# Kernel tuning notes

Measured on AMD Instinct MI355X. Metric: run time of the kernel, lower is better.

The kernel has to match this reference:

```python
import jax, jax.numpy as jnp
import numpy as np

N = 20000
E = 320000
IN_DIM = 16
H = 128
HEADS = 4
NEG_SLOPE = 0.2  # GATv2Conv default
EPS_LN = 1e-5


def setup_inputs() -> dict:
    key = jax.random.key(0)
    ks = jax.random.split(key, 16)
    f32 = jnp.float32
    def rn(k, shape, scale):
        return jax.random.normal(k, shape, dtype=f32) * scale
    s_in = 1.0 / np.sqrt(IN_DIM)
    s_h = 1.0 / np.sqrt(H)
    s_4h = 1.0 / np.sqrt(4 * H)
    s_2h = 1.0 / np.sqrt(2 * H)
    inp = {}
    inp["x"] = jax.random.normal(ks[0], (N, IN_DIM), dtype=f32)
    inp["edge_index"] = jax.random.randint(ks[1], (2, E), 0, N)
    inp["edge_attr"] = jax.random.normal(ks[2], (E, 2), dtype=f32)
    inp["emb_w"] = rn(ks[3], (IN_DIM, H), s_in)
    inp["emb_b"] = jnp.zeros((H,), f32)
    # 3 GATv2 layers stacked on leading axis
    inp["lin_l"] = rn(ks[4], (3, H, HEADS * H), s_h)
    inp["lin_r"] = rn(ks[5], (3, H, HEADS * H), s_h)
    inp["lin_edge"] = rn(ks[6], (3, 2, HEADS * H), 1.0 / np.sqrt(2.0))
    inp["att"] = rn(ks[7], (3, HEADS, H), s_h)
    inp["conv_bias01"] = jnp.zeros((2, HEADS * H), f32)  # concat=True layers
    inp["conv_bias2"] = jnp.zeros((H,), f32)             # concat=False layer
    inp["proj_w"] = rn(ks[8], (2, HEADS * H, H), s_4h)
    inp["proj_b"] = jnp.zeros((2, H), f32)
    inp["n1_g"] = jnp.ones((3, H), f32)
    inp["n1_b"] = jnp.zeros((3, H), f32)
    inp["n2_g"] = jnp.ones((3, H), f32)
    inp["n2_b"] = jnp.zeros((3, H), f32)
    inp["ffn_w1"] = rn(ks[9], (3, H, 2 * H), s_h)
    inp["ffn_b1"] = jnp.zeros((3, 2 * H), f32)
    inp["ffn_w2"] = rn(ks[10], (3, 2 * H, H), s_2h)
    inp["ffn_b2"] = jnp.zeros((3, H), f32)
    return inp


def layer_norm(x, g, b):
    mu = jnp.mean(x, axis=-1, keepdims=True)
    var = jnp.mean((x - mu) ** 2, axis=-1, keepdims=True)
    return (x - mu) * jax.lax.rsqrt(var + EPS_LN) * g + b


def gatv2(h, src, dst, eattr, Wl, Wr, We, att, bias, concat, n):
    # h: [n, H]; per-edge gather -> GATv2 attention -> segment softmax -> scatter-add
    xl = (h @ Wl).reshape(n, HEADS, H)   # source transform
    xr = (h @ Wr).reshape(n, HEADS, H)   # target transform
    ee = (eattr @ We).reshape(-1, HEADS, H)
    e = jax.nn.leaky_relu(xl[src] + xr[dst] + ee, NEG_SLOPE)  # [E', HEADS, H]
    score = jnp.einsum('ehc,hc->eh', e, att)                  # [E', HEADS]
    smax = jax.ops.segment_max(score, dst, num_segments=n)
    p = jnp.exp(score - smax[dst])
    denom = jax.ops.segment_sum(p, dst, num_segments=n)
    alpha = p / (denom[dst] + 1e-16)
    out = jax.ops.segment_sum(xl[src] * alpha[..., None], dst, num_segments=n)
    if concat:
        return out.reshape(n, HEADS * H) + bias
    return jnp.mean(out, axis=1) + bias


def reference(x, edge_index, edge_attr, emb_w, emb_b, lin_l, lin_r, lin_edge, att,
              conv_bias01, conv_bias2, proj_w, proj_b, n1_g, n1_b, n2_g, n2_b,
              ffn_w1, ffn_b1, ffn_w2, ffn_b2):
    n = x.shape[0]
    e = edge_attr.shape[0]
    # PyG add_self_loops with fill_value='mean': self-loop attr = mean of incoming edge attrs
    ones = jnp.ones((e,), x.dtype)
    deg = jax.ops.segment_sum(ones, edge_index[1], num_segments=n)
    loop_attr = jax.ops.segment_sum(edge_attr, edge_index[1], num_segments=n) / jnp.maximum(deg, 1.0)[:, None]
    ar = jnp.arange(n)
    src = jnp.concatenate([edge_index[0], ar])
    dst = jnp.concatenate([edge_index[1], ar])
    ea = jnp.concatenate([edge_attr, loop_attr], axis=0)

    h = x @ emb_w + emb_b
    for i in range(3):
        concat = i < 2
        bias = conv_bias01[i] if concat else conv_bias2
        h_in = h
        h = gatv2(h, src, dst, ea, lin_l[i], lin_r[i], lin_edge[i], att[i], bias, concat, n)
        if concat:
            h = h @ proj_w[i] + proj_b[i]
        h = layer_norm(h + h_in, n1_g[i], n1_b[i])
        h2 = h
        h = jax.nn.gelu(h @ ffn_w1[i] + ffn_b1[i], approximate=False) @ ffn_w2[i] + ffn_b2[i]
        h = layer_norm(h + h2, n2_g[i], n2_b[i])
    return h
```

## Files before the change

kernel.cpp:

```cpp
#include <hip/hip_runtime.h>
#include <math.h>

#define IN_DIM 16
#define HDIM   128
#define HEADS  4
#define HH     512
#define FFH    256
#define NEG_SLOPE 0.2f

typedef _Float16 half8 __attribute__((ext_vector_type(8)));
typedef _Float16 h8 __attribute__((ext_vector_type(8)));
typedef _Float16 h4 __attribute__((ext_vector_type(4)));
typedef _Float16 h2 __attribute__((ext_vector_type(2)));
typedef float f32x4 __attribute__((ext_vector_type(4)));
typedef int i32x4 __attribute__((ext_vector_type(4)));

struct __align__(8) Edge { int src; _Float16 ea0, ea1; };

static __device__ inline float hsum8(h8 v) {
    h4 a = __builtin_shufflevector(v, v, 0, 1, 2, 3) +
           __builtin_shufflevector(v, v, 4, 5, 6, 7);
    h2 b = __builtin_shufflevector(a, a, 0, 1) +
           __builtin_shufflevector(a, a, 2, 3);
    return (float)b[0] + (float)b[1];
}

static __device__ inline h8 shfl_xor_h8(h8 v, int off) {
    union { h8 h; i32x4 i; } u;
    u.h = v;
    u.i.x = __shfl_xor(u.i.x, off);
    u.i.y = __shfl_xor(u.i.y, off);
    u.i.z = __shfl_xor(u.i.z, off);
    u.i.w = __shfl_xor(u.i.w, off);
    return u.h;
}

__global__ void xpad_kernel(const float* __restrict__ x, _Float16* __restrict__ xh, int n) {
    int idx = blockIdx.x * 256 + threadIdx.x;
    if (idx >= n * 64) return;
    int r = idx >> 6, k = idx & 63;
    xh[idx] = (k < IN_DIM) ? (_Float16)x[r * IN_DIM + k] : (_Float16)0.0f;
}

struct WDesc { const float* src; _Float16* dst; int Ksrc; int lgKd; int lgN; };
struct WDescs { WDesc d[15]; };
__global__ void wconv_kernel(WDescs ds) {
    WDesc w = ds.d[blockIdx.y];
    int Kd = 1 << w.lgKd;
    int total = 1 << (w.lgKd + w.lgN);
    for (int idx = blockIdx.x * 256 + threadIdx.x; idx < total; idx += gridDim.x * 256) {
        int n2 = idx >> w.lgKd, k = idx & (Kd - 1);
        w.dst[idx] = (k < w.Ksrc) ? (_Float16)w.src[(k << w.lgN) + n2] : (_Float16)0.0f;
    }
}

__global__ void wcvt_kernel(const float* __restrict__ we, const float* __restrict__ att,
                            const float* __restrict__ cb,
                            _Float16* __restrict__ weh, _Float16* __restrict__ atth,
                            _Float16* __restrict__ cbh) {
    int i = blockIdx.x * 256 + threadIdx.x;
    if (i < 3072) weh[i] = (_Float16)we[i];
    else if (i < 4608) atth[i - 3072] = (_Float16)att[i - 3072];
    else if (i < 5632) cbh[i - 4608] = (_Float16)cb[i - 4608];
}

__global__ void deg_kernel(const int* __restrict__ ei, const float* __restrict__ eattr,
                           float* deg, float* asum, int E) {
    int e = blockIdx.x * blockDim.x + threadIdx.x;
    if (e >= E) return;
    int d = ei[E + e];
    atomicAdd(&deg[d], 1.0f);
    atomicAdd(&asum[2 * d], eattr[2 * e]);
    atomicAdd(&asum[2 * d + 1], eattr[2 * e + 1]);
}

__global__ void scan_kernel(const float* __restrict__ deg, int* row_ptr, int* cur, int n) {
    __shared__ int sums[1024];
    int tid = threadIdx.x;
    int per = (n + 1023) / 1024;
    int s0 = tid * per;
    int s1 = s0 + per; if (s1 > n) s1 = n;
    int s = 0;
    for (int i = s0; i < s1; i++) s += (int)deg[i] + 1;
    int mysum = s;
    sums[tid] = s;
    __syncthreads();
    for (int dd = 1; dd < 1024; dd <<= 1) {
        int t = (tid >= dd) ? sums[tid - dd] : 0;
        __syncthreads();
        sums[tid] += t;
        __syncthreads();
    }
    int run = sums[tid] - mysum;
    for (int i = s0; i < s1; i++) {
        row_ptr[i] = run; cur[i] = run;
        run += (int)deg[i] + 1;
    }
    if (tid == 1023) row_ptr[n] = sums[1023];
}

__global__ void scatter_kernel(const int* __restrict__ ei, const float* __restrict__ eattr,
                               const float* __restrict__ deg, const float* __restrict__ asum,
                               int* cur, Edge* csr, int E, int n) {
    int i = blockIdx.x * blockDim.x + threadIdx.x;
    if (i >= E + n) return;
    Edge ed;
    int pos;
    if (i < E) {
        int d = ei[E + i];
        pos = atomicAdd(&cur[d], 1);
        ed.src = ei[i];
        ed.ea0 = (_Float16)eattr[2 * i];
        ed.ea1 = (_Float16)eattr[2 * i + 1];
    } else {
        int nd = i - E;
        float dv = fmaxf(deg[nd], 1.0f);
        pos = atomicAdd(&cur[nd], 1);
        ed.src = nd;
        ed.ea0 = (_Float16)(asum[2 * nd] / dv);
        ed.ea1 = (_Float16)(asum[2 * nd + 1] / dv);
    }
    csr[pos] = ed;
}

template <int KT, int OUTMODE>
__global__ __launch_bounds__(256) void gemm_bstat(const _Float16* __restrict__ A, int lda,
                                                  const _Float16* __restrict__ BT,
                                                  const float* __restrict__ bias,
                                                  float* __restrict__ C32,
                                                  _Float16* __restrict__ C16,
                                                  int M, int Nstride, int numMT) {
    const int PAD = 8, KC = KT / 32;
    __shared__ _Float16 Bs[128][KT + PAD];
    int tid = threadIdx.x;
    int wave = tid >> 6, lane = tid & 63;
    int quad = lane >> 4, l16 = lane & 15;
    int wrow = (wave >> 1) * 32, wcol = (wave & 1) * 64;
    int n0 = blockIdx.x * 128;

#pragma unroll
    for (int t = 0; t < KT / 16; t++) {
        int idx = tid + t * 256;
        int r = idx / (KT / 8), kb = (idx % (KT / 8)) * 8;
        *(half8*)&Bs[r][kb] = *(const half8*)(BT + (size_t)(n0 + r) * KT + kb);
    }
    __syncthreads();

    half8 bfrag[4][KC];
#pragma unroll
    for (int j = 0; j < 4; j++)
#pragma unroll
        for (int kc = 0; kc < KC; kc++)
            bfrag[j][kc] = *(const half8*)&Bs[wcol + j * 16 + l16][kc * 32 + quad * 8];

    float biasj[4];
#pragma unroll
    for (int j = 0; j < 4; j++)
        biasj[j] = bias ? bias[n0 + wcol + j * 16 + l16] : 0.0f;

    for (int mt = blockIdx.y; mt < numMT; mt += gridDim.y) {
        int rbase = mt * 64 + wrow;
        half8 af[2][KC];
#pragma unroll
        for (int i = 0; i < 2; i++) {
            int row = rbase + i * 16 + l16;
#pragma unroll
            for (int kc = 0; kc < KC; kc++)
                af[i][kc] = (row < M) ? *(const half8*)(A + (size_t)row * lda + kc * 32 + quad * 8)
                                      : (half8)(_Float16)0.0f;
        }
        f32x4 acc[2][4] = {};
#pragma unroll
        for (int kc = 0; kc < KC; kc++)
#pragma unroll
            for (int i = 0; i < 2; i++)
#pragma unroll
                for (int j = 0; j < 4; j++)
                    acc[i][j] = __builtin_amdgcn_mfma_f32_16x16x32_f16(af[i][kc], bfrag[j][kc], acc[i][j], 0, 0, 0);
#pragma unroll
        for (int i = 0; i < 2; i++) {
#pragma unroll
            for (int r = 0; r < 4; r++) {
                int row = rbase + i * 16 + quad * 4 + r;
                if (row >= M) continue;
#pragma unroll
                for (int j = 0; j < 4; j++) {
                    int col = n0 + wcol + j * 16 + l16;
                    float v = acc[i][j][r] + biasj[j];
                    if (OUTMODE == 2)
                        C32[(size_t)row * Nstride + col] = v;
                    C16[(size_t)row * Nstride + col] = (_Float16)v;
                }
            }
        }
    }
}

__global__ __launch_bounds__(256) void gemm_ln(const _Float16* __restrict__ A, int lda,
                                               const _Float16* __restrict__ BT,
                                               const float* __restrict__ bias,
                                               const float* __restrict__ R,
                                               const float* __restrict__ g,
                                               const float* __restrict__ b,
                                               float* __restrict__ C32,
                                               _Float16* __restrict__ C16,
                                               int M, int K) {
    const int BK = 64, PAD = 8;
    __shared__ _Float16 As[64][BK + PAD];
    __shared__ _Float16 Bs[128][BK + PAD];
    int tid = threadIdx.x;
    int wave = tid >> 6, lane = tid & 63;
    int quad = lane >> 4, l16 = lane & 15;
    int mBase = blockIdx.x * 64;

    f32x4 acc[8] = {};

    for (int k0 = 0; k0 < K; k0 += BK) {
#pragma unroll
        for (int t = 0; t < 2; t++) {
            int idx = tid + t * 256;
            int r = idx >> 3, kb = (idx & 7) * 8;
            half8 hv = {};
            int grow = mBase + r;
            if (grow < M) hv = *(const half8*)(A + (size_t)grow * lda + k0 + kb);
            *(half8*)&As[r][kb] = hv;
        }
#pragma unroll
        for (int t = 0; t < 4; t++) {
            int idx = tid + t * 256;
            int r = idx >> 3, kb = (idx & 7) * 8;
            *(half8*)&Bs[r][kb] = *(const half8*)(BT + (size_t)r * K + k0 + kb);
        }
        __syncthreads();
#pragma unroll
        for (int kc = 0; kc < 2; kc++) {
            half8 a = *(const half8*)&As[wave * 16 + l16][kc * 32 + quad * 8];
#pragma unroll
            for (int j = 0; j < 8; j++) {
                half8 bb = *(const half8*)&Bs[j * 16 + l16][kc * 32 + quad * 8];
                acc[j] = __builtin_amdgcn_mfma_f32_16x16x32_f16(a, bb, acc[j], 0, 0, 0);
            }
        }
        __syncthreads();
    }

    float gj[8], bj[8], biasj[8];
#pragma unroll
    for (int j = 0; j < 8; j++) {
        int col = j * 16 + l16;
        biasj[j] = bias[col];
        gj[j] = g[col];
        bj[j] = b[col];
    }
    int row0 = mBase + wave * 16 + quad * 4;
    float sum[4] = {}, sq[4] = {};
#pragma unroll
    for (int r = 0; r < 4; r++) {
        int row = row0 + r;
        bool ok = row < M;
        size_t base = (size_t)row * HDIM;
#pragma unroll
        for (int j = 0; j < 8; j++) {
            float v = acc[j][r] + biasj[j] + (ok ? R[base + j * 16 + l16] : 0.0f);
            acc[j][r] = v;
            sum[r] += v;
            sq[r] += v * v;
        }
    }
#pragma unroll
    for (int r = 0; r < 4; r++) {
#pragma unroll
        for (int off = 1; off < 16; off <<= 1) {
            sum[r] += __shfl_xor(sum[r], off);
            sq[r] += __shfl_xor(sq[r], off);
        }
    }
#pragma unroll
    for (int r = 0; r < 4; r++) {
        int row = row0 + r;
        if (row >= M) continue;
        size_t base = (size_t)row * HDIM;
        float mu = sum[r] * (1.0f / HDIM);
        float var = sq[r] * (1.0f / HDIM) - mu * mu;
        float invstd = rsqrtf(var + 1e-5f);
#pragma unroll
        for (int j = 0; j < 8; j++) {
            float o = (acc[j][r] - mu) * invstd * gj[j] + bj[j];
            C32[base + j * 16 + l16] = o;
            if (C16) C16[base + j * 16 + l16] = (_Float16)o;
        }
    }
}

__global__ __launch_bounds__(256) void ffn_fused(const _Float16* __restrict__ A,
                                                 const _Float16* __restrict__ W1T,
                                                 const float* __restrict__ b1,
                                                 const _Float16* __restrict__ W2T,
                                                 const float* __restrict__ b2,
                                                 const float* __restrict__ R,
                                                 const float* __restrict__ g,
                                                 const float* __restrict__ b,
                                                 float* __restrict__ C32,
                                                 _Float16* __restrict__ C16,
                                                 int M) {
    __shared__ _Float16 Ws[128][128 + 8];
    __shared__ _Float16 Mid[64][256 + 8];
    int tid = threadIdx.x;
    int wave = tid >> 6, lane = tid & 63;
    int quad = lane >> 4, l16 = lane & 15;
    int mBase = blockIdx.x * 64;

    half8 afrag[4];
    {
        int row = mBase + wave * 16 + l16;
#pragma unroll
        for (int kc = 0; kc < 4; kc++) {
            if (row < M)
                afrag[kc] = *(const half8*)(A + (size_t)row * HDIM + kc * 32 + quad * 8);
            else
                afrag[kc] = (half8)(_Float16)0.0f;
        }
    }

#pragma unroll
    for (int h = 0; h < 2; h++) {
        if (h) __syncthreads();
#pragma unroll
        for (int t = 0; t < 8; t++) {
            int idx = tid + t * 256;
            int r = idx >> 4, kb = (idx & 15) * 8;
            *(half8*)&Ws[r][kb] = *(const half8*)(W1T + (size_t)(h * 128 + r) * HDIM + kb);
        }
        __syncthreads();
        f32x4 acc[8] = {};
#pragma unroll
        for (int kc = 0; kc < 4; kc++) {
#pragma unroll
            for (int j = 0; j < 8; j++) {
                half8 bb = *(const half8*)&Ws[j * 16 + l16][kc * 32 + quad * 8];
                acc[j] = __builtin_amdgcn_mfma_f32_16x16x32_f16(afrag[kc], bb, acc[j], 0, 0, 0);
            }
        }
#pragma unroll
        for (int j = 0; j < 8; j++) {
            float bj1 = b1[h * 128 + j * 16 + l16];
#pragma unroll
            for (int r = 0; r < 4; r++) {
                float v = acc[j][r] + bj1;
                v = 0.5f * v * (1.0f + erff(v * 0.70710678118654752f));
                Mid[wave * 16 + quad * 4 + r][h * 128 + j * 16 + l16] = (_Float16)v;
            }
        }
    }
    __syncthreads();

    f32x4 acc2[8] = {};
#pragma unroll
    for (int kc2 = 0; kc2 < 2; kc2++) {
        if (kc2) __syncthreads();
#pragma unroll
        for (int t = 0; t < 8; t++) {
            int idx = tid + t * 256;
            int r = idx >> 4, kb = (idx & 15) * 8;
            *(half8*)&Ws[r][kb] = *(const half8*)(W2T + (size_t)r * FFH + kc2 * 128 + kb);
        }
        __syncthreads();
#pragma unroll
        for (int kc = 0; kc < 4; kc++) {
            half8 am = *(const half8*)&Mid[wave * 16 + l16][kc2 * 128 + kc * 32 + quad * 8];
#pragma unroll
            for (int j = 0; j < 8; j++) {
                half8 bb = *(const half8*)&Ws[j * 16 + l16][kc * 32 + quad * 8];
                acc2[j] = __builtin_amdgcn_mfma_f32_16x16x32_f16(am, bb, acc2[j], 0, 0, 0);
            }
        }
    }

    float gj[8], bj[8], b2j[8];
#pragma unroll
    for (int j = 0; j < 8; j++) {
        int col = j * 16 + l16;
        b2j[j] = b2[col];
        gj[j] = g[col];
        bj[j] = b[col];
    }
    int row0 = mBase + wave * 16 + quad * 4;
    float sum[4] = {}, sq[4] = {};
#pragma unroll
    for (int r = 0; r < 4; r++) {
        int row = row0 + r;
        bool ok = row < M;
        size_t base = (size_t)row * HDIM;
#pragma unroll
        for (int j = 0; j < 8; j++) {
            float v = acc2[j][r] + b2j[j] + (ok ? R[base + j * 16 + l16] : 0.0f);
            acc2[j][r] = v;
            sum[r] += v;
            sq[r] += v * v;
        }
    }
#pragma unroll
    for (int r = 0; r < 4; r++) {
#pragma unroll
        for (int off = 1; off < 16; off <<= 1) {
            sum[r] += __shfl_xor(sum[r], off);
            sq[r] += __shfl_xor(sq[r], off);
        }
    }
#pragma unroll
    for (int r = 0; r < 4; r++) {
        int row = row0 + r;
        if (row >= M) continue;
        size_t base = (size_t)row * HDIM;
        float mu = sum[r] * (1.0f / HDIM);
        float var = sq[r] * (1.0f / HDIM) - mu * mu;
        float invstd = rsqrtf(var + 1e-5f);
#pragma unroll
        for (int j = 0; j < 8; j++) {
            float o = (acc2[j][r] - mu) * invstd * gj[j] + bj[j];
            C32[base + j * 16 + l16] = o;
            if (C16) C16[base + j * 16 + l16] = (_Float16)o;
        }
    }
}

__global__ __launch_bounds__(256) void gat_edge_kernel(
    const _Float16* __restrict__ XLR,
    const int* __restrict__ row_ptr, const Edge* __restrict__ csr,
    const _Float16* __restrict__ WEH,
    const _Float16* __restrict__ ATTH,
    const _Float16* __restrict__ CBH,
    const float* __restrict__ cb2,
    _Float16* __restrict__ OUT16, float* __restrict__ OUT32,
    const float* __restrict__ R, const float* __restrict__ lng,
    const float* __restrict__ lnb, _Float16* __restrict__ OUT16h,
    int n, int concat) {
    int tid = threadIdx.x;
    int wave = tid >> 6, lane = tid & 63;
    int g = lane >> 5;
    int sub = lane & 31;
    int node = blockIdx.x * 4 + wave;
    if (node >= n) return;
    int c0 = sub * 16;

    h8 w0[2], w1[2], att[2], xr[2], acc[2];
#pragma unroll
    for (int k = 0; k < 2; k++) {
        w0[k]  = *(const h8*)(WEH + c0 + k * 8);
        w1[k]  = *(const h8*)(WEH + 512 + c0 + k * 8);
        att[k] = *(const h8*)(ATTH + c0 + k * 8);
        acc[k] = (h8)(_Float16)0.0f;
    }
    const _Float16 slope = (_Float16)NEG_SLOPE;

    {
        unsigned nb = ((unsigned)node << 10) + 512u + (unsigned)c0;
        xr[0] = *(const h8*)(XLR + nb);
        xr[1] = *(const h8*)(XLR + nb + 8);
    }

    float m = -1e30f, l = 0.0f;
    int beg = row_ptr[node], end = row_ptr[node + 1];
    int e = beg + g;

    for (; e + 2 < end; e += 4) {
        Edge eg0 = csr[e], eg1 = csr[e + 2];
        unsigned r0 = ((unsigned)eg0.src << 10) + (unsigned)c0;
        unsigned r1 = ((unsigned)eg1.src << 10) + (unsigned)c0;
        h8 x0a = *(const h8*)(XLR + r0);
        h8 x0b = *(const h8*)(XLR + r0 + 8);
        h8 x1a = *(const h8*)(XLR + r1);
        h8 x1b = *(const h8*)(XLR + r1 + 8);

        h8 v;
        h8 p80, p81;
        v = x0a + (xr[0] + w0[0] * eg0.ea0 + w1[0] * eg0.ea1);
        v = __builtin_elementwise_max(v, v * slope);
        p80 = v * att[0];
        v = x0b + (xr[1] + w0[1] * eg0.ea0 + w1[1] * eg0.ea1);
        v = __builtin_elementwise_max(v, v * slope);
        p80 += v * att[1];
        v = x1a + (xr[0] + w0[0] * eg1.ea0 + w1[0] * eg1.ea1);
        v = __builtin_elementwise_max(v, v * slope);
        p81 = v * att[0];
        v = x1b + (xr[1] + w0[1] * eg1.ea0 + w1[1] * eg1.ea1);
        v = __builtin_elementwise_max(v, v * slope);
        p81 += v * att[1];

        float p0 = hsum8(p80);
        float p1 = hsum8(p81);
        p0 += __shfl_xor(p0, 1); p1 += __shfl_xor(p1, 1);
        p0 += __shfl_xor(p0, 2); p1 += __shfl_xor(p1, 2);
        p0 += __shfl_xor(p0, 4); p1 += __shfl_xor(p1, 4);

        float mnew = fmaxf(m, fmaxf(p0, p1));
        float sc  = __expf(m - mnew);
        float e0f = __expf(p0 - mnew);
        float e1f = __expf(p1 - mnew);
        l = l * sc + e0f + e1f;
        _Float16 hs = (_Float16)sc, h0 = (_Float16)e0f, h1 = (_Float16)e1f;
        acc[0] = acc[0] * hs + x0a * h0 + x1a * h1;
        acc[1] = acc[1] * hs + x0b * h0 + x1b * h1;
        m = mnew;
    }
    for (; e < end; e += 2) {
        Edge eg0 = csr[e];
        unsigned r0 = ((unsigned)eg0.src << 10) + (unsigned)c0;
        h8 x0a = *(const h8*)(XLR + r0);
        h8 x0b = *(const h8*)(XLR + r0 + 8);
        h8 v;
        h8 p80;
        v = x0a + (xr[0] + w0[0] * eg0.ea0 + w1[0] * eg0.ea1);
        v = __builtin_elementwise_max(v, v * slope);
        p80 = v * att[0];
        v = x0b + (xr[1] + w0[1] * eg0.ea0 + w1[1] * eg0.ea1);
        v = __builtin_elementwise_max(v, v * slope);
        p80 += v * att[1];
        float p0 = hsum8(p80);
        p0 += __shfl_xor(p0, 1);
        p0 += __shfl_xor(p0, 2);
        p0 += __shfl_xor(p0, 4);
        float mnew = fmaxf(m, p0);
        float sc  = __expf(m - mnew);
        float e0f = __expf(p0 - mnew);
        l = l * sc + e0f;
        _Float16 hs = (_Float16)sc, h0 = (_Float16)e0f;
        acc[0] = acc[0] * hs + x0a * h0;
        acc[1] = acc[1] * hs + x0b * h0;
        m = mnew;
    }

    {
        float m2 = __shfl_xor(m, 32);
        float l2 = __shfl_xor(l, 32);
        h8 a20 = shfl_xor_h8(acc[0], 32);
        h8 a21 = shfl_xor_h8(acc[1], 32);
        float mS = fmaxf(m, m2);
        float sA = __expf(m - mS);
        float sB = __expf(m2 - mS);
        l = l * sA + l2 * sB;
        _Float16 hA = (_Float16)sA, hB = (_Float16)sB;
        acc[0] = acc[0] * hA + a20 * hB;
        acc[1] = acc[1] * hA + a21 * hB;
    }

    float invf = 1.0f / (l + 1e-16f);
    if (concat) {
        _Float16 hi = (_Float16)invf;
        h8 o0 = acc[0] * hi + *(const h8*)(CBH + c0);
        h8 o1 = acc[1] * hi + *(const h8*)(CBH + c0 + 8);
        if (g == 0) {
            unsigned ob = ((unsigned)node << 10) + (unsigned)c0;
            *(h8*)(OUT16 + ob) = o0;
            *(h8*)(OUT16 + ob + 8) = o1;
        }
    } else {
        _Float16 hi = (_Float16)invf;
        h8 t0 = acc[0] * hi;
        h8 t1 = acc[1] * hi;
        t0 = t0 + shfl_xor_h8(t0, 8);
        t1 = t1 + shfl_xor_h8(t1, 8);
        t0 = t0 + shfl_xor_h8(t0, 16);
        t1 = t1 + shfl_xor_h8(t1, 16);
        if (g == 0 && sub < 8) {
            int d0 = sub * 16;
            const float* Rp = R + (size_t)node * HDIM + d0;
            const float* cp = cb2 + d0;
            float v[16];
            float sum = 0.0f, sq = 0.0f;
#pragma unroll
            for (int q = 0; q < 4; q++) {
                f32x4 rv = *(const f32x4*)(Rp + q * 4);
                f32x4 cv = *(const f32x4*)(cp + q * 4);
#pragma unroll
                for (int t = 0; t < 4; t++) {
                    int k2 = q * 4 + t;
                    float base = (k2 < 8) ? (float)t0[k2 & 7] : (float)t1[k2 & 7];
                    float vv = base * 0.25f + cv[t] + rv[t];
                    v[k2] = vv;
                    sum += vv;
                    sq += vv * vv;
                }
            }
            sum += __shfl_xor(sum, 1); sq += __shfl_xor(sq, 1);
            sum += __shfl_xor(sum, 2); sq += __shfl_xor(sq, 2);
            sum += __shfl_xor(sum, 4); sq += __shfl_xor(sq, 4);
            float mu = sum * (1.0f / HDIM);
            float var = sq * (1.0f / HDIM) - mu * mu;
            float invstd = rsqrtf(var + 1e-5f);
            float* op = OUT32 + (size_t)node * HDIM + d0;
            _Float16* oh = OUT16h + (size_t)node * HDIM + d0;
            _Float16 o16[16];
#pragma unroll
            for (int q = 0; q < 4; q++) {
                f32x4 gv = *(const f32x4*)(lng + d0 + q * 4);
                f32x4 bv = *(const f32x4*)(lnb + d0 + q * 4);
                f32x4 ov;
#pragma unroll
                for (int t = 0; t < 4; t++) {
                    float o = (v[q * 4 + t] - mu) * invstd * gv[t] + bv[t];
                    ov[t] = o;
                    o16[q * 4 + t] = (_Float16)o;
                }
                *(f32x4*)(op + q * 4) = ov;
            }
            *(h8*)(oh) = *(h8*)&o16[0];
            *(h8*)(oh + 8) = *(h8*)&o16[8];
        }
    }
}

extern "C" void kernel_launch(void* const* d_in, const int* in_sizes, int n_in,
                              void* d_out, int out_size, void* d_ws, size_t ws_size,
                              hipStream_t stream) {
    const float* x        = (const float*)d_in[0];
    const int*   ei       = (const int*)d_in[1];
    const float* eattr    = (const float*)d_in[2];
    const float* emb_w    = (const float*)d_in[3];
    const float* emb_b    = (const float*)d_in[4];
    const float* lin_l    = (const float*)d_in[5];
    const float* lin_r    = (const float*)d_in[6];
    const float* lin_edge = (const float*)d_in[7];
    const float* attw     = (const float*)d_in[8];
    const float* cb01     = (const float*)d_in[9];
    const float* cb2      = (const float*)d_in[10];
    const float* proj_w   = (const float*)d_in[11];
    const float* proj_b   = (const float*)d_in[12];
    const float* n1g      = (const float*)d_in[13];
    const float* n1b      = (const float*)d_in[14];
    const float* n2g      = (const float*)d_in[15];
    const float* n2b      = (const float*)d_in[16];
    const float* fw1      = (const float*)d_in[17];
    const float* fb1      = (const float*)d_in[18];
    const float* fw2      = (const float*)d_in[19];
    const float* fb2      = (const float*)d_in[20];
    float* out = (float*)d_out;

    const int n = in_sizes[0] / IN_DIM;
    const int E = in_sizes[2] / 2;
    const int EP = E + n;
    const int numMT = (n + 63) / 64;

    size_t off = 0;
    auto alloc = [&](size_t bytes) {
        void* p = (char*)d_ws + off;
        off += (bytes + 255) & ~(size_t)255;
        return p;
    };
    float* deg     = (float*)alloc((size_t)n * 4);
    float* asum    = (float*)alloc((size_t)2 * n * 4);
    int*   row_ptr = (int*)alloc((size_t)(n + 1) * 4);
    int*   cur     = (int*)alloc((size_t)n * 4);
    Edge*  csr     = (Edge*)alloc((size_t)EP * 8);
    float* H0      = (float*)alloc((size_t)n * HDIM * 4);
    float* H1      = (float*)alloc((size_t)n * HDIM * 4);
    _Float16* H0h  = (_Float16*)alloc((size_t)n * HDIM * 2);
    _Float16* H1h  = (_Float16*)alloc((size_t)n * HDIM * 2);
    _Float16* XLR  = (_Float16*)alloc((size_t)n * 1024 * 2);
    _Float16* xh   = (_Float16*)alloc((size_t)n * 64 * 2);
    _Float16* wt_emb  = (_Float16*)alloc((size_t)HDIM * 64 * 2);
    _Float16* wt_llr  = (_Float16*)alloc((size_t)3 * 1024 * HDIM * 2);
    _Float16* wt_proj = (_Float16*)alloc((size_t)2 * HDIM * HH * 2);
    _Float16* wt_f1   = (_Float16*)alloc((size_t)3 * FFH * HDIM * 2);
    _Float16* wt_f2   = (_Float16*)alloc((size_t)3 * HDIM * FFH * 2);
    _Float16* weh     = (_Float16*)alloc((size_t)3 * 1024 * 2);
    _Float16* atth    = (_Float16*)alloc((size_t)3 * 512 * 2);
    _Float16* cbh     = (_Float16*)alloc((size_t)2 * 512 * 2);
    (void)ws_size;

    xpad_kernel<<<(n * 64 + 255) / 256, 256, 0, stream>>>(x, xh, n);
    WDescs ds;
    int di = 0;
    ds.d[di++] = {emb_w, wt_emb, IN_DIM, 6, 7};
    for (int i = 0; i < 3; i++) {
        ds.d[di++] = {lin_l + (size_t)i * HDIM * HH, wt_llr + (size_t)i * 1024 * HDIM, HDIM, 7, 9};
        ds.d[di++] = {lin_r + (size_t)i * HDIM * HH, wt_llr + (size_t)i * 1024 * HDIM + (size_t)512 * HDIM, HDIM, 7, 9};
    }
    for (int i = 0; i < 2; i++)
        ds.d[di++] = {proj_w + (size_t)i * HH * HDIM, wt_proj + (size_t)i * HDIM * HH, HH, 9, 7};
    for (int i = 0; i < 3; i++)
        ds.d[di++] = {fw1 + (size_t)i * HDIM * FFH, wt_f1 + (size_t)i * FFH * HDIM, HDIM, 7, 8};
    for (int i = 0; i < 3; i++)
        ds.d[di++] = {fw2 + (size_t)i * FFH * HDIM, wt_f2 + (size_t)i * HDIM * FFH, FFH, 8, 7};
    wconv_kernel<<<dim3(32, 15), 256, 0, stream>>>(ds);
    wcvt_kernel<<<22, 256, 0, stream>>>(lin_edge, attw, cb01, weh, atth, cbh);

    (void)hipMemsetAsync(deg, 0, (size_t)n * 4, stream);
    (void)hipMemsetAsync(asum, 0, (size_t)2 * n * 4, stream);
    deg_kernel<<<(E + 255) / 256, 256, 0, stream>>>(ei, eattr, deg, asum, E);
    scan_kernel<<<1, 1024, 0, stream>>>(deg, row_ptr, cur, n);
    scatter_kernel<<<(EP + 255) / 256, 256, 0, stream>>>(ei, eattr, deg, asum, cur, csr, E, n);

    gemm_bstat<64, 2><<<dim3(1, numMT), 256, 0, stream>>>(
        xh, 64, wt_emb, emb_b, H0, H0h, n, HDIM, numMT);

    for (int i = 0; i < 3; i++) {
        int concat = (i < 2);
        gemm_bstat<128, 1><<<dim3(8, 80), 256, 0, stream>>>(
            H0h, HDIM, wt_llr + (size_t)i * 1024 * HDIM, nullptr,
            nullptr, XLR, n, 1024, numMT);
        gat_edge_kernel<<<(n + 3) / 4, 256, 0, stream>>>(
            XLR, row_ptr, csr,
            weh + (size_t)i * 1024, atth + (size_t)i * 512,
            concat ? (cbh + (size_t)i * 512) : nullptr, cb2,
            XLR + 512, H1,
            H0, n1g + (size_t)i * HDIM, n1b + (size_t)i * HDIM, H1h,
            n, concat);
        if (concat) {
            gemm_ln<<<(n + 63) / 64, 256, 0, stream>>>(
                XLR + 512, 1024, wt_proj + (size_t)i * HDIM * HH,
                proj_b + (size_t)i * HDIM, H0,
                n1g + (size_t)i * HDIM, n1b + (size_t)i * HDIM,
                H1, H1h, n, HH);
        }
        float* lnout = (i == 2) ? out : H0;
        _Float16* lnout16 = (i == 2) ? nullptr : H0h;
        ffn_fused<<<(n + 63) / 64, 256, 0, stream>>>(
            H1h, wt_f1 + (size_t)i * FFH * HDIM, fb1 + (size_t)i * FFH,
            wt_f2 + (size_t)i * HDIM * FFH, fb2 + (size_t)i * HDIM, H1,
            n2g + (size_t)i * HDIM, n2b + (size_t)i * HDIM,
            lnout, lnout16, n);
    }
}
```

Baseline: 564.6 us.

## Merge prep kernels, combine memsets, use nontemporal stores/loads for streamed data

Folds the input-pad, weight-convert and small-parameter-convert kernels into one prep kernel launch, and merges the two memsets into one contiguous memset that assumes deg and asum sit next to each other in the workspace. It also switches the fp16 GEMM outputs, the GAT self-row loads and the GAT outputs to nontemporal loads and stores. The aim is to cut launch overhead and keep streamed data from polluting cache. The catch is that XLR is gathered right after it is written, so nontemporal stores there may lose useful L2 residency.

```diff
diff --git a/kernel.cpp b/kernel.cpp
--- a/kernel.cpp
+++ b/kernel.cpp
@@ -35,33 +35,35 @@
     return u.h;
 }
 
-__global__ void xpad_kernel(const float* __restrict__ x, _Float16* __restrict__ xh, int n) {
-    int idx = blockIdx.x * 256 + threadIdx.x;
-    if (idx >= n * 64) return;
-    int r = idx >> 6, k = idx & 63;
-    xh[idx] = (k < IN_DIM) ? (_Float16)x[r * IN_DIM + k] : (_Float16)0.0f;
-}
-
 struct WDesc { const float* src; _Float16* dst; int Ksrc; int lgKd; int lgN; };
 struct WDescs { WDesc d[15]; };
-__global__ void wconv_kernel(WDescs ds) {
-    WDesc w = ds.d[blockIdx.y];
-    int Kd = 1 << w.lgKd;
-    int total = 1 << (w.lgKd + w.lgN);
-    for (int idx = blockIdx.x * 256 + threadIdx.x; idx < total; idx += gridDim.x * 256) {
-        int n2 = idx >> w.lgKd, k = idx & (Kd - 1);
-        w.dst[idx] = (k < w.Ksrc) ? (_Float16)w.src[(k << w.lgN) + n2] : (_Float16)0.0f;
-    }
-}
-
-__global__ void wcvt_kernel(const float* __restrict__ we, const float* __restrict__ att,
+__global__ void prep_kernel(WDescs ds,
+                            const float* __restrict__ x, _Float16* __restrict__ xh, int n,
+                            const float* __restrict__ we, const float* __restrict__ att,
                             const float* __restrict__ cb,
                             _Float16* __restrict__ weh, _Float16* __restrict__ atth,
                             _Float16* __restrict__ cbh) {
-    int i = blockIdx.x * 256 + threadIdx.x;
-    if (i < 3072) weh[i] = (_Float16)we[i];
-    else if (i < 4608) atth[i - 3072] = (_Float16)att[i - 3072];
-    else if (i < 5632) cbh[i - 4608] = (_Float16)cb[i - 4608];
+    int y = blockIdx.y;
+    if (y < 15) {
+        WDesc w = ds.d[y];
+        int Kd = 1 << w.lgKd;
+        int total = 1 << (w.lgKd + w.lgN);
+        for (int idx = blockIdx.x * 256 + threadIdx.x; idx < total; idx += gridDim.x * 256) {
+            int n2 = idx >> w.lgKd, k = idx & (Kd - 1);
+            w.dst[idx] = (k < w.Ksrc) ? (_Float16)w.src[(k << w.lgN) + n2] : (_Float16)0.0f;
+        }
+    } else if (y == 15) {
+        int total = n * 64;
+        for (int idx = blockIdx.x * 256 + threadIdx.x; idx < total; idx += gridDim.x * 256) {
+            int r = idx >> 6, k = idx & 63;
+            xh[idx] = (k < IN_DIM) ? (_Float16)x[r * IN_DIM + k] : (_Float16)0.0f;
+        }
+    } else {
+        int i = blockIdx.x * 256 + threadIdx.x;
+        if (i < 3072) weh[i] = (_Float16)we[i];
+        else if (i < 4608) atth[i - 3072] = (_Float16)att[i - 3072];
+        else if (i < 5632) cbh[i - 4608] = (_Float16)cb[i - 4608];
+    }
 }
 
 __global__ void deg_kernel(const int* __restrict__ ei, const float* __restrict__ eattr,
@@ -187,9 +189,12 @@
                 for (int j = 0; j < 4; j++) {
                     int col = n0 + wcol + j * 16 + l16;
                     float v = acc[i][j][r] + biasj[j];
-                    if (OUTMODE == 2)
+                    if (OUTMODE == 2) {
                         C32[(size_t)row * Nstride + col] = v;
-                    C16[(size_t)row * Nstride + col] = (_Float16)v;
+                        C16[(size_t)row * Nstride + col] = (_Float16)v;
+                    } else {
+                        __builtin_nontemporal_store((_Float16)v, &C16[(size_t)row * Nstride + col]);
+                    }
                 }
             }
         }
@@ -455,8 +460,8 @@
 
     {
         unsigned nb = ((unsigned)node << 10) + 512u + (unsigned)c0;
-        xr[0] = *(const h8*)(XLR + nb);
-        xr[1] = *(const h8*)(XLR + nb + 8);
+        xr[0] = __builtin_nontemporal_load((const h8*)(XLR + nb));
+        xr[1] = __builtin_nontemporal_load((const h8*)(XLR + nb + 8));
     }
 
     float m = -1e30f, l = 0.0f;
@@ -551,8 +556,8 @@
         h8 o1 = acc[1] * hi + *(const h8*)(CBH + c0 + 8);
         if (g == 0) {
             unsigned ob = ((unsigned)node << 10) + (unsigned)c0;
-            *(h8*)(OUT16 + ob) = o0;
-            *(h8*)(OUT16 + ob + 8) = o1;
+            __builtin_nontemporal_store(o0, (h8*)(OUT16 + ob));
+            __builtin_nontemporal_store(o1, (h8*)(OUT16 + ob + 8));
         }
     } else {
         _Float16 hi = (_Float16)invf;
@@ -602,10 +607,10 @@
                     ov[t] = o;
                     o16[q * 4 + t] = (_Float16)o;
                 }
-                *(f32x4*)(op + q * 4) = ov;
+                __builtin_nontemporal_store(ov, (f32x4*)(op + q * 4));
             }
-            *(h8*)(oh) = *(h8*)&o16[0];
-            *(h8*)(oh + 8) = *(h8*)&o16[8];
+            __builtin_nontemporal_store(*(h8*)&o16[0], (h8*)(oh));
+            __builtin_nontemporal_store(*(h8*)&o16[8], (h8*)(oh + 8));
         }
     }
 }
@@ -668,7 +673,6 @@
     _Float16* cbh     = (_Float16*)alloc((size_t)2 * 512 * 2);
     (void)ws_size;
 
-    xpad_kernel<<<(n * 64 + 255) / 256, 256, 0, stream>>>(x, xh, n);
     WDescs ds;
     int di = 0;
     ds.d[di++] = {emb_w, wt_emb, IN_DIM, 6, 7};
@@ -682,11 +686,10 @@
         ds.d[di++] = {fw1 + (size_t)i * HDIM * FFH, wt_f1 + (size_t)i * FFH * HDIM, HDIM, 7, 8};
     for (int i = 0; i < 3; i++)
         ds.d[di++] = {fw2 + (size_t)i * FFH * HDIM, wt_f2 + (size_t)i * HDIM * FFH, FFH, 8, 7};
-    wconv_kernel<<<dim3(32, 15), 256, 0, stream>>>(ds);
-    wcvt_kernel<<<22, 256, 0, stream>>>(lin_edge, attw, cb01, weh, atth, cbh);
-
-    (void)hipMemsetAsync(deg, 0, (size_t)n * 4, stream);
-    (void)hipMemsetAsync(asum, 0, (size_t)2 * n * 4, stream);
+    prep_kernel<<<dim3(64, 17), 256, 0, stream>>>(ds, x, xh, n,
+                                                  lin_edge, attw, cb01, weh, atth, cbh);
+
+    (void)hipMemsetAsync(deg, 0, (size_t)((char*)asum - (char*)deg) + (size_t)2 * n * 4, stream);
     deg_kernel<<<(E + 255) / 256, 256, 0, stream>>>(ei, eattr, deg, asum, E);
     scan_kernel<<<1, 1024, 0, stream>>>(deg, row_ptr, cur, n);
     scatter_kernel<<<(EP + 255) / 256, 256, 0, stream>>>(ei, eattr, deg, asum, cur, csr, E, n);
```

Measured after the change: 586.7 us. +3.9%, slower.
